# Kernel tuning notes

Hardware: AMD Instinct MI355X
Metric: run time of the kernel (lower is better)

Reference implementation:

```python
import jax, jax.numpy as jnp
import numpy as np

NUM_CLASSES = 80
M = 50.0  # MAX_ANOT_ANCHOR_POSITION_DISTANCE
ALPHA = 0.25
GAMMA = 2.0
EPS = 1e-4


def setup_inputs() -> dict:
    key = jax.random.key(0)
    k1, k2, k3, k4, k5 = jax.random.split(key, 5)
    B, N, C, K = 8, 100000, NUM_CLASSES, 32
    classifications = jax.random.uniform(k1, (B, N, C), dtype=jnp.float32,
                                         minval=0.01, maxval=0.99)
    regressions = jax.random.normal(k2, (B, N, 3), dtype=jnp.float32)
    # anchors: x,y in [0,1000), alpha in [0, 2*pi)
    axy = jax.random.uniform(k3, (1, N, 2), dtype=jnp.float32) * 1000.0
    aal = jax.random.uniform(k3, (1, N, 1), dtype=jnp.float32) * 6.2831853
    anchors = jnp.concatenate([axy, aal], axis=-1)
    gxy = jax.random.uniform(k4, (B, K, 2), dtype=jnp.float32) * 1000.0
    gal = jax.random.uniform(k4, (B, K, 1), dtype=jnp.float32) * 6.2831853
    lab = jax.random.randint(k5, (B, K, 1), 0, C).astype(jnp.float32)
    annotations = jnp.concatenate([gxy, gal, lab], axis=-1)
    return {"classifications": classifications, "regressions": regressions,
            "anchors": anchors, "annotations": annotations}


def _per_image(cls_p, reg, anchor, ann):
    # cls_p: [N,C], reg: [N,3], anchor: [N,3], ann: [K,4]
    C = cls_p.shape[1]
    cls_p = jnp.clip(cls_p, EPS, 1.0 - EPS)
    # distance [N,K] = 10*sqrt(dx^2+dy^2) + |dalpha|
    dx = anchor[:, 0:1] - ann[None, :, 0]
    dy = anchor[:, 1:2] - ann[None, :, 1]
    da = jnp.abs(anchor[:, 2:3] - ann[None, :, 2])
    dist = 10.0 * jnp.sqrt(dx * dx + dy * dy) + da
    dmin = jnp.min(dist, axis=1)          # [N]
    amin = jnp.argmin(dist, axis=1)       # [N]
    pos = dmin <= 11.0 * M                # [N]
    neg = dmin >= 13.0 * M                # [N]
    assigned = ann[amin]                  # [N,4]
    labels = assigned[:, 3].astype(jnp.int32)
    onehot = jax.nn.one_hot(labels, C, dtype=jnp.bool_)
    targets = jnp.where((neg | pos)[:, None], 0.0, -1.0)   # [N,C]
    targets = jnp.where(pos[:, None] & onehot, 1.0, targets)
    is_pos_t = targets == 1.0
    alpha_f = jnp.where(is_pos_t, ALPHA, 1.0 - ALPHA)
    focal_w = alpha_f * jnp.where(is_pos_t, 1.0 - cls_p, cls_p) ** GAMMA
    bce = -(targets * jnp.log(cls_p) + (1.0 - targets) * jnp.log(1.0 - cls_p))
    cls_loss = jnp.where(targets != -1.0, focal_w * bce, 0.0)
    num_pos = jnp.sum(pos.astype(jnp.float32))
    cls_l = jnp.sum(cls_loss) / jnp.maximum(num_pos, 1.0)
    tgt = assigned[:, :3] - anchor                     # [N,3]
    diff_xy = jnp.abs(tgt[:, :2] - reg[:, :2])         # [N,2]
    diff_ang = 1.0 - jnp.cos(tgt[:, 2] - reg[:, 2])    # [N]
    lxy = jnp.where(diff_xy <= 1.0 / 9.0,
                    0.5 * 9.0 * diff_xy * diff_xy,
                    diff_xy - 0.5 / 9.0)
    posf = pos.astype(jnp.float32)
    denom = jnp.maximum(num_pos, 1.0)
    reg_l = jnp.sum(lxy * posf[:, None]) / (2.0 * denom) \
          + jnp.sum(diff_ang * posf) / denom
    reg_l = jnp.where(num_pos > 0, reg_l, 0.0)
    return cls_l, reg_l


def reference(classifications, regressions, anchors, annotations):
    anchor = anchors[0]  # [N,3]
    cls_ls, reg_ls = jax.vmap(_per_image, in_axes=(0, 0, None, 0))(
        classifications, regressions, anchor, annotations)
    return (jnp.mean(cls_ls, keepdims=True), jnp.mean(reg_ls, keepdims=True))
```

## Files before the change

kernel.cpp:

```cpp
#include <hip/hip_runtime.h>

#define NUM_CLASSES 80
#define K_ANN 32
#define NF4 (NUM_CLASSES / 4)
#define TILE 512
#define ITER (TILE * NF4 / 256)
#define UNROLL 4
#define PREF 4

typedef float f32x4 __attribute__((ext_vector_type(4)));


__global__ __launch_bounds__(256, 8) void focal_main(
    const float* __restrict__ cls,
    const float* __restrict__ reg,
    const float* __restrict__ anc,
    const float* __restrict__ ann,
    float* __restrict__ ws,
    int N, int nblk)
{
    const int b  = blockIdx.y;
    const int bx = blockIdx.x;
    const int t  = threadIdx.x;
    const int n0 = bx * TILE;
    const bool full = (n0 + TILE <= N);

    __shared__ f32x4  s_pref[PREF * 256];
    __shared__ float4 s_ann4[K_ANN];
    __shared__ float  s_g[TILE];

    if (t < K_ANN)
        s_ann4[t] = ((const float4*)(ann + (long long)b * K_ANN * 4))[t];

    const f32x4* __restrict__ base =
        (const f32x4*)(cls + ((long long)b * N + n0) * NUM_CLASSES);

    if (full) {
        const int wid = t >> 6;
        #pragma unroll
        for (int u = 0; u < PREF; ++u)
            __builtin_amdgcn_global_load_lds(
                (const __attribute__((address_space(1))) unsigned int*)&base[u * 256 + t],
                (__attribute__((address_space(3))) unsigned int*)&s_pref[u * 256 + wid * 64],
                16, 0, 0);
    }
    __syncthreads();

    float csum = 0.f, npos = 0.f, rxy = 0.f, rang = 0.f;

    {
        const int n1 = n0 + t;
        const int n2 = n0 + 256 + t;
        const bool ok1 = n1 < N, ok2 = n2 < N;
        const int m1 = ok1 ? n1 : N - 1;
        const int m2 = ok2 ? n2 : N - 1;
        const float ax1 = anc[m1 * 3 + 0], ay1 = anc[m1 * 3 + 1], aa1 = anc[m1 * 3 + 2];
        const float ax2 = anc[m2 * 3 + 0], ay2 = anc[m2 * 3 + 1], aa2 = anc[m2 * 3 + 2];

        float d1 = 1e30f, d2 = 1e30f;
        int   k1 = 0,     k2 = 0;
        #pragma unroll 4
        for (int k = 0; k < K_ANN; ++k) {
            const float4 a4 = s_ann4[k];
            {
                const float dx = ax1 - a4.x, dy = ay1 - a4.y;
                const float da = fabsf(aa1 - a4.z);
                const float d  = fmaf(10.f, sqrtf(fmaf(dx, dx, dy * dy)), da);
                if (d < d1) { d1 = d; k1 = k; }
            }
            {
                const float dx = ax2 - a4.x, dy = ay2 - a4.y;
                const float da = fabsf(aa2 - a4.z);
                const float d  = fmaf(10.f, sqrtf(fmaf(dx, dx, dy * dy)), da);
                if (d < d2) { d2 = d; k2 = k; }
            }
        }

        #pragma unroll
        for (int r = 0; r < 2; ++r) {
            const bool  ok   = r ? ok2 : ok1;
            const int   n    = r ? n2  : n1;
            const float dmin = r ? d2  : d1;
            const int   kmin = r ? k2  : k1;
            const float ax   = r ? ax2 : ax1;
            const float ay   = r ? ay2 : ay1;
            const float aa   = r ? aa2 : aa1;

            const bool pos = ok && (dmin <= 550.f);
            const bool neg = ok && (dmin >= 650.f);
            s_g[r * 256 + t] = (pos | neg) ? 0.75f : 0.f;

            if (pos) {
                const float4 a4 = s_ann4[kmin];
                const float tx = a4.x - ax, ty = a4.y - ay, tz = a4.z - aa;
                const float* rp = reg + ((long long)b * N + n) * 3;
                const float dxr = fabsf(tx - rp[0]);
                const float dyr = fabsf(ty - rp[1]);
                rxy += ((dxr <= 1.f / 9.f) ? 4.5f * dxr * dxr : dxr - 0.5f / 9.f)
                     + ((dyr <= 1.f / 9.f) ? 4.5f * dyr * dyr : dyr - 0.5f / 9.f);
                rang += 1.f - __cosf(tz - rp[2]);
                npos += 1.f;

                const int lab = (int)a4.w;
                const float p = cls[((long long)b * N + n) * NUM_CLASSES + lab];
                csum += 0.75f * p * p * __logf(1.f - p)
                      - 0.25f * (1.f - p) * (1.f - p) * __logf(p);
            }
        }
    }
    __syncthreads();

    float acc = 0.f;
    if (full) {
        #pragma unroll
        for (int u = 0; u < PREF; ++u) {
            const unsigned idx = (unsigned)(u * 256 + t);
            const float g = s_g[idx / 20u];
            const f32x4 v = s_pref[idx];
            float s4 = 0.f;
            s4 = fmaf(v.x * v.x, __logf(1.f - v.x), s4);
            s4 = fmaf(v.y * v.y, __logf(1.f - v.y), s4);
            s4 = fmaf(v.z * v.z, __logf(1.f - v.z), s4);
            s4 = fmaf(v.w * v.w, __logf(1.f - v.w), s4);
            acc = fmaf(g, s4, acc);
        }
        #pragma unroll 1
        for (int i0 = PREF; i0 < ITER; i0 += UNROLL) {
            f32x4 v[UNROLL];
            #pragma unroll
            for (int u = 0; u < UNROLL; ++u)
                v[u] = base[(i0 + u) * 256 + t];
            __builtin_amdgcn_sched_barrier(0);
            #pragma unroll
            for (int u = 0; u < UNROLL; ++u) {
                const unsigned idx = (unsigned)((i0 + u) * 256 + t);
                const float g = s_g[idx / 20u];
                float s4 = 0.f;
                s4 = fmaf(v[u].x * v[u].x, __logf(1.f - v[u].x), s4);
                s4 = fmaf(v[u].y * v[u].y, __logf(1.f - v[u].y), s4);
                s4 = fmaf(v[u].z * v[u].z, __logf(1.f - v[u].z), s4);
                s4 = fmaf(v[u].w * v[u].w, __logf(1.f - v[u].w), s4);
                acc = fmaf(g, s4, acc);
            }
        }
    } else {
        const int total4 = (N - n0) * NF4;
        for (int i = t; i < total4; i += 256) {
            const float g = s_g[(unsigned)i / 20u];
            const f32x4 v = base[i];
            float s4 = 0.f;
            s4 = fmaf(v.x * v.x, __logf(1.f - v.x), s4);
            s4 = fmaf(v.y * v.y, __logf(1.f - v.y), s4);
            s4 = fmaf(v.z * v.z, __logf(1.f - v.z), s4);
            s4 = fmaf(v.w * v.w, __logf(1.f - v.w), s4);
            acc = fmaf(g, s4, acc);
        }
    }
    csum -= acc;

    #pragma unroll
    for (int off = 32; off > 0; off >>= 1) {
        csum += __shfl_down(csum, off);
        npos += __shfl_down(npos, off);
        rxy  += __shfl_down(rxy , off);
        rang += __shfl_down(rang, off);
    }
    __shared__ float s_red[4][4];
    const int wid = t >> 6;
    if ((t & 63) == 0) {
        s_red[wid][0] = csum; s_red[wid][1] = npos;
        s_red[wid][2] = rxy;  s_red[wid][3] = rang;
    }
    __syncthreads();
    if (t == 0) {
        float a0 = 0.f, a1 = 0.f, a2 = 0.f, a3 = 0.f;
        #pragma unroll
        for (int w = 0; w < 4; ++w) {
            a0 += s_red[w][0]; a1 += s_red[w][1];
            a2 += s_red[w][2]; a3 += s_red[w][3];
        }
        float4* slot = (float4*)(ws + ((long long)b * nblk + bx) * 4);
        *slot = make_float4(a0, a1, a2, a3);
    }
}

__global__ __launch_bounds__(512) void focal_final(
    const float* __restrict__ ws, float* __restrict__ out, int B, int nblk)
{
    const int t    = threadIdx.x;
    const int b    = t >> 6;
    const int lane = t & 63;

    float a0 = 0.f, a1 = 0.f, a2 = 0.f, a3 = 0.f;
    if (b < B) {
        for (int i = lane; i < nblk; i += 64) {
            const float4 v = *(const float4*)(ws + ((long long)b * nblk + i) * 4);
            a0 += v.x; a1 += v.y; a2 += v.z; a3 += v.w;
        }
    }
    #pragma unroll
    for (int off = 32; off > 0; off >>= 1) {
        a0 += __shfl_down(a0, off);
        a1 += __shfl_down(a1, off);
        a2 += __shfl_down(a2, off);
        a3 += __shfl_down(a3, off);
    }

    __shared__ float s_cl[8], s_rl[8];
    if (lane == 0 && b < B) {
        const float den = fmaxf(a1, 1.f);
        s_cl[b] = a0 / den;
        const float r = a2 / (2.f * den) + a3 / den;
        s_rl[b] = (a1 > 0.f) ? r : 0.f;
    }
    __syncthreads();
    if (t == 0) {
        float cl = 0.f, rl = 0.f;
        for (int i = 0; i < B; ++i) { cl += s_cl[i]; rl += s_rl[i]; }
        out[0] = cl / (float)B;
        out[1] = rl / (float)B;
    }
}

extern "C" void kernel_launch(void* const* d_in, const int* in_sizes, int n_in,
                              void* d_out, int out_size, void* d_ws, size_t ws_size,
                              hipStream_t stream)
{
    (void)n_in; (void)out_size; (void)ws_size;
    const float* cls = (const float*)d_in[0];
    const float* reg = (const float*)d_in[1];
    const float* anc = (const float*)d_in[2];
    const float* ann = (const float*)d_in[3];
    float* out = (float*)d_out;
    float* ws  = (float*)d_ws;

    const int N = in_sizes[2] / 3;
    const int B = in_sizes[3] / (K_ANN * 4);
    const int nblk = (N + TILE - 1) / TILE;

    dim3 grid(nblk, B);
    focal_main<<<grid, dim3(256), 0, stream>>>(cls, reg, anc, ann, ws, N, nblk);
    focal_final<<<1, dim3(512), 0, stream>>>(ws, out, B, nblk);
}
```

Measured before the change: 60.04 us.

## Skip class loads for ignored anchors, fold ln2 into weight, shrink tile

For anchors in the ignore band (weight zero), the class-probability vector loads are redirected to an address that is already cached, which cuts HBM traffic for that band. The natural log becomes log2, with ln2 folded into the per-anchor weight constant. The regression loads are hoisted ahead of the distance loop, and TILE drops from 512 to 448, which adds a remainder loop for the unroll. The risks are divergent addresses within a wavefront, more blocks to schedule, and a saving that depends on what fraction of anchors fall in the ignore band.

```diff
diff --git a/kernel.cpp b/kernel.cpp
--- a/kernel.cpp
+++ b/kernel.cpp
@@ -3,7 +3,7 @@
 #define NUM_CLASSES 80
 #define K_ANN 32
 #define NF4 (NUM_CLASSES / 4)
-#define TILE 512
+#define TILE 448
 #define ITER (TILE * NF4 / 256)
 #define UNROLL 4
 #define PREF 4
@@ -36,12 +36,12 @@
         (const f32x4*)(cls + ((long long)b * N + n0) * NUM_CLASSES);
 
     if (full) {
-        const int wid = t >> 6;
+        const int wid0 = t >> 6;
         #pragma unroll
         for (int u = 0; u < PREF; ++u)
             __builtin_amdgcn_global_load_lds(
                 (const __attribute__((address_space(1))) unsigned int*)&base[u * 256 + t],
-                (__attribute__((address_space(3))) unsigned int*)&s_pref[u * 256 + wid * 64],
+                (__attribute__((address_space(3))) unsigned int*)&s_pref[u * 256 + wid0 * 64],
                 16, 0, 0);
     }
     __syncthreads();
@@ -51,11 +51,18 @@
     {
         const int n1 = n0 + t;
         const int n2 = n0 + 256 + t;
-        const bool ok1 = n1 < N, ok2 = n2 < N;
+        const bool ok1 = n1 < N;
+        const bool ok2 = (t < TILE - 256) && (n2 < N);
         const int m1 = ok1 ? n1 : N - 1;
         const int m2 = ok2 ? n2 : N - 1;
         const float ax1 = anc[m1 * 3 + 0], ay1 = anc[m1 * 3 + 1], aa1 = anc[m1 * 3 + 2];
         const float ax2 = anc[m2 * 3 + 0], ay2 = anc[m2 * 3 + 1], aa2 = anc[m2 * 3 + 2];
+        const float r01 = reg[((long long)b * N + m1) * 3 + 0];
+        const float r11 = reg[((long long)b * N + m1) * 3 + 1];
+        const float r21 = reg[((long long)b * N + m1) * 3 + 2];
+        const float r02 = reg[((long long)b * N + m2) * 3 + 0];
+        const float r12 = reg[((long long)b * N + m2) * 3 + 1];
+        const float r22 = reg[((long long)b * N + m2) * 3 + 2];
 
         float d1 = 1e30f, d2 = 1e30f;
         int   k1 = 0,     k2 = 0;
@@ -85,20 +92,23 @@
             const float ax   = r ? ax2 : ax1;
             const float ay   = r ? ay2 : ay1;
             const float aa   = r ? aa2 : aa1;
+            const float rr0  = r ? r02 : r01;
+            const float rr1  = r ? r12 : r11;
+            const float rr2  = r ? r22 : r21;
 
             const bool pos = ok && (dmin <= 550.f);
             const bool neg = ok && (dmin >= 650.f);
-            s_g[r * 256 + t] = (pos | neg) ? 0.75f : 0.f;
+            if (r == 0 || t < TILE - 256)
+                s_g[r * 256 + t] = (pos | neg) ? 0.51986038f : 0.f;
 
             if (pos) {
                 const float4 a4 = s_ann4[kmin];
                 const float tx = a4.x - ax, ty = a4.y - ay, tz = a4.z - aa;
-                const float* rp = reg + ((long long)b * N + n) * 3;
-                const float dxr = fabsf(tx - rp[0]);
-                const float dyr = fabsf(ty - rp[1]);
+                const float dxr = fabsf(tx - rr0);
+                const float dyr = fabsf(ty - rr1);
                 rxy += ((dxr <= 1.f / 9.f) ? 4.5f * dxr * dxr : dxr - 0.5f / 9.f)
                      + ((dyr <= 1.f / 9.f) ? 4.5f * dyr * dyr : dyr - 0.5f / 9.f);
-                rang += 1.f - __cosf(tz - rp[2]);
+                rang += 1.f - __cosf(tz - rr2);
                 npos += 1.f;
 
                 const int lab = (int)a4.w;
@@ -118,41 +128,58 @@
             const float g = s_g[idx / 20u];
             const f32x4 v = s_pref[idx];
             float s4 = 0.f;
-            s4 = fmaf(v.x * v.x, __logf(1.f - v.x), s4);
-            s4 = fmaf(v.y * v.y, __logf(1.f - v.y), s4);
-            s4 = fmaf(v.z * v.z, __logf(1.f - v.z), s4);
-            s4 = fmaf(v.w * v.w, __logf(1.f - v.w), s4);
+            s4 = fmaf(v.x * v.x, __log2f(1.f - v.x), s4);
+            s4 = fmaf(v.y * v.y, __log2f(1.f - v.y), s4);
+            s4 = fmaf(v.z * v.z, __log2f(1.f - v.z), s4);
+            s4 = fmaf(v.w * v.w, __log2f(1.f - v.w), s4);
             acc = fmaf(g, s4, acc);
         }
         #pragma unroll 1
-        for (int i0 = PREF; i0 < ITER; i0 += UNROLL) {
-            f32x4 v[UNROLL];
+        for (int i0 = PREF; i0 + UNROLL <= ITER; i0 += UNROLL) {
+            unsigned ix[UNROLL];
+            float    g [UNROLL];
+            f32x4    v [UNROLL];
+            #pragma unroll
+            for (int u = 0; u < UNROLL; ++u) {
+                ix[u] = (unsigned)((i0 + u) * 256 + t);
+                g[u]  = s_g[ix[u] / 20u];
+            }
             #pragma unroll
             for (int u = 0; u < UNROLL; ++u)
-                v[u] = base[(i0 + u) * 256 + t];
+                v[u] = base[(g[u] != 0.f) ? ix[u] : (unsigned)t];
             __builtin_amdgcn_sched_barrier(0);
             #pragma unroll
             for (int u = 0; u < UNROLL; ++u) {
-                const unsigned idx = (unsigned)((i0 + u) * 256 + t);
-                const float g = s_g[idx / 20u];
                 float s4 = 0.f;
-                s4 = fmaf(v[u].x * v[u].x, __logf(1.f - v[u].x), s4);
-                s4 = fmaf(v[u].y * v[u].y, __logf(1.f - v[u].y), s4);
-                s4 = fmaf(v[u].z * v[u].z, __logf(1.f - v[u].z), s4);
-                s4 = fmaf(v[u].w * v[u].w, __logf(1.f - v[u].w), s4);
-                acc = fmaf(g, s4, acc);
-            }
+                s4 = fmaf(v[u].x * v[u].x, __log2f(1.f - v[u].x), s4);
+                s4 = fmaf(v[u].y * v[u].y, __log2f(1.f - v[u].y), s4);
+                s4 = fmaf(v[u].z * v[u].z, __log2f(1.f - v[u].z), s4);
+                s4 = fmaf(v[u].w * v[u].w, __log2f(1.f - v[u].w), s4);
+                acc = fmaf(g[u], s4, acc);
+            }
+        }
+        #pragma unroll
+        for (int i0 = PREF + ((ITER - PREF) / UNROLL) * UNROLL; i0 < ITER; ++i0) {
+            const unsigned idx = (unsigned)(i0 * 256 + t);
+            const float g = s_g[idx / 20u];
+            const f32x4 v = base[(g != 0.f) ? idx : (unsigned)t];
+            float s4 = 0.f;
+            s4 = fmaf(v.x * v.x, __log2f(1.f - v.x), s4);
+            s4 = fmaf(v.y * v.y, __log2f(1.f - v.y), s4);
+            s4 = fmaf(v.z * v.z, __log2f(1.f - v.z), s4);
+            s4 = fmaf(v.w * v.w, __log2f(1.f - v.w), s4);
+            acc = fmaf(g, s4, acc);
         }
     } else {
         const int total4 = (N - n0) * NF4;
         for (int i = t; i < total4; i += 256) {
             const float g = s_g[(unsigned)i / 20u];
-            const f32x4 v = base[i];
+            const f32x4 v = base[(g != 0.f) ? i : t];
             float s4 = 0.f;
-            s4 = fmaf(v.x * v.x, __logf(1.f - v.x), s4);
-            s4 = fmaf(v.y * v.y, __logf(1.f - v.y), s4);
-            s4 = fmaf(v.z * v.z, __logf(1.f - v.z), s4);
-            s4 = fmaf(v.w * v.w, __logf(1.f - v.w), s4);
+            s4 = fmaf(v.x * v.x, __log2f(1.f - v.x), s4);
+            s4 = fmaf(v.y * v.y, __log2f(1.f - v.y), s4);
+            s4 = fmaf(v.z * v.z, __log2f(1.f - v.z), s4);
+            s4 = fmaf(v.w * v.w, __log2f(1.f - v.w), s4);
             acc = fmaf(g, s4, acc);
         }
     }
```

New measurement: 51.94 us. 1.16x faster.
